# Performance work log

Measured on AMD Instinct MI355X. Metric: run time of the kernel, lower is better.

The kernel has to match this reference:

```python
import jax, jax.numpy as jnp
import numpy as np

N_NODES = 50000
N_EDGES = 800000
IN_F, HID, NCLS = 128, 64, 64
N_EXTRA = 2          # layer - 2
K_STEPS = 10
ALPHA = 0.1
BN_EPS = 1e-5


def setup_inputs() -> dict:
    key = jax.random.key(0)
    ks = jax.random.split(key, 20)
    d = {}
    d['x'] = jax.random.normal(ks[0], (N_NODES, IN_F), dtype=jnp.float32)
    d['edge_index'] = jax.random.randint(ks[1], (2, N_EDGES), 0, N_NODES, dtype=jnp.int64)
    s = 1.0 / np.sqrt(HID)
    d['W1'] = jax.random.normal(ks[2], (IN_F, HID), dtype=jnp.float32) / np.sqrt(IN_F)
    d['b1'] = jnp.zeros((HID,), jnp.float32)
    d['W2'] = jax.random.normal(ks[3], (HID, HID), dtype=jnp.float32) * s
    d['b2'] = jnp.zeros((HID,), jnp.float32)
    d['Wx'] = jax.random.normal(ks[4], (N_EXTRA, HID, HID), dtype=jnp.float32) * s
    d['bx'] = jnp.zeros((N_EXTRA, HID), jnp.float32)
    d['g1'] = jnp.ones((HID,), jnp.float32); d['be1'] = jnp.zeros((HID,), jnp.float32)
    d['g2'] = jnp.ones((HID,), jnp.float32); d['be2'] = jnp.zeros((HID,), jnp.float32)
    d['g3'] = jnp.ones((HID,), jnp.float32); d['be3'] = jnp.zeros((HID,), jnp.float32)
    d['Wfc'] = jax.random.normal(ks[5], (HID, NCLS), dtype=jnp.float32) * s
    d['bfc'] = jnp.zeros((NCLS,), jnp.float32)
    return d


def _gcn_norm(edge_index, n):
    # add self-loops, symmetric D^-1/2 (A+I) D^-1/2 normalization (PyG GCNConv default)
    loop = jnp.arange(n, dtype=edge_index.dtype)
    src = jnp.concatenate([edge_index[0], loop])
    dst = jnp.concatenate([edge_index[1], loop])
    deg = jax.ops.segment_sum(jnp.ones(src.shape[0], jnp.float32), dst, num_segments=n)
    dinv = jnp.where(deg > 0, jax.lax.rsqrt(deg), 0.0)
    return src, dst, dinv[src] * dinv[dst]


def _propagate(x, src, dst, w, n):
    # gather-scale-scatter: out[dst] += w * x[src]
    return jax.ops.segment_sum(x[src] * w[:, None], dst, num_segments=n)


def _bn(x, g, b):
    # BatchNorm1d in training mode: batch statistics over the node dim
    m = jnp.mean(x, axis=0)
    v = jnp.var(x, axis=0)
    return g * (x - m) * jax.lax.rsqrt(v + BN_EPS) + b


def reference(x, edge_index, W1, b1, W2, b2, Wx, bx, g1, be1, g2, be2, g3, be3, Wfc, bfc):
    n = x.shape[0]
    src, dst, w = _gcn_norm(edge_index, n)
    h = _propagate(x @ W1, src, dst, w, n) + b1
    h = jax.nn.relu(_bn(h, g1, be1))
    h = _propagate(h @ W2, src, dst, w, n) + b2
    h = jax.nn.relu(_bn(h, g2, be2))
    for i in range(Wx.shape[0]):
        h = _propagate(h @ Wx[i], src, dst, w, n) + bx[i]
        h = jax.nn.relu(_bn(h, g3, be3))
    # APPNP: K power-iteration steps with teleport back to h0
    h0 = h
    for _ in range(K_STEPS):
        h = (1.0 - ALPHA) * _propagate(h, src, dst, w, n) + ALPHA * h0
    out = h @ Wfc + bfc
    return jax.nn.log_softmax(out, axis=1)
```

## Files before the change

### kernel.cpp

```cpp
#include <hip/hip_runtime.h>
#include <hip/hip_fp16.h>
#include <cstdint>
#include <cstddef>

#define NN 50000
#define NE 800000
#define HID 64
#define INF_ 128
#define BN_EPS 1e-5f
#define NGRP (NN / 8)
#define NG16 (NN / 16)
#define SCAN_B 196
#define NSLICE 32
#define NBKT 16

typedef float floatx2 __attribute__((ext_vector_type(2)));

__device__ __forceinline__ float4 h8_to_f4(float2 raw) {
    union { float f; __half2 h; } ua, ub;
    ua.f = raw.x; ub.f = raw.y;
    float2 fa = __half22float2(ua.h), fb = __half22float2(ub.h);
    return make_float4(fa.x, fa.y, fb.x, fb.y);
}
__device__ __forceinline__ float2 f4_to_h8(float4 v) {
    union { float f; __half2 h; } ua, ub;
    ua.h = __float22half2_rn(make_float2(v.x, v.y));
    ub.h = __float22half2_rn(make_float2(v.z, v.w));
    return make_float2(ua.f, ub.f);
}
struct f8 { float v[8]; };
__device__ __forceinline__ f8 h16_to_f8(float4 raw) {
    f8 r;
    union { float f; __half2 h; } u;
    float2 a;
    u.f = raw.x; a = __half22float2(u.h); r.v[0] = a.x; r.v[1] = a.y;
    u.f = raw.y; a = __half22float2(u.h); r.v[2] = a.x; r.v[3] = a.y;
    u.f = raw.z; a = __half22float2(u.h); r.v[4] = a.x; r.v[5] = a.y;
    u.f = raw.w; a = __half22float2(u.h); r.v[6] = a.x; r.v[7] = a.y;
    return r;
}
__device__ __forceinline__ float4 f8_to_h16(const f8& s) {
    union { float f; __half2 h; } u;
    float4 o;
    u.h = __float22half2_rn(make_float2(s.v[0], s.v[1])); o.x = u.f;
    u.h = __float22half2_rn(make_float2(s.v[2], s.v[3])); o.y = u.f;
    u.h = __float22half2_rn(make_float2(s.v[4], s.v[5])); o.z = u.f;
    u.h = __float22half2_rn(make_float2(s.v[6], s.v[7])); o.w = u.f;
    return o;
}

__device__ __forceinline__ void fp8x8_to_f(unsigned lo, unsigned hi, float out[8]) {
    floatx2 a = __builtin_amdgcn_cvt_pk_f32_fp8((int)lo, false);
    floatx2 b = __builtin_amdgcn_cvt_pk_f32_fp8((int)lo, true);
    floatx2 c = __builtin_amdgcn_cvt_pk_f32_fp8((int)hi, false);
    floatx2 d = __builtin_amdgcn_cvt_pk_f32_fp8((int)hi, true);
    out[0] = a[0]; out[1] = a[1]; out[2] = b[0]; out[3] = b[1];
    out[4] = c[0]; out[5] = c[1]; out[6] = d[0]; out[7] = d[1];
}
__device__ __forceinline__ void fp8x16_to_f(uint4 r, float out[16]) {
    fp8x8_to_f(r.x, r.y, out);
    fp8x8_to_f(r.z, r.w, out + 8);
}
__device__ __forceinline__ uint2 f_to_fp8x8(const float v[8]) {
    int w0 = __builtin_amdgcn_cvt_pk_fp8_f32(v[0], v[1], 0, false);
    w0 = __builtin_amdgcn_cvt_pk_fp8_f32(v[2], v[3], w0, true);
    int w1 = __builtin_amdgcn_cvt_pk_fp8_f32(v[4], v[5], 0, false);
    w1 = __builtin_amdgcn_cvt_pk_fp8_f32(v[6], v[7], w1, true);
    uint2 o; o.x = (unsigned)w0; o.y = (unsigned)w1;
    return o;
}
__device__ __forceinline__ uint4 f_to_fp8x16(const float v[16]) {
    uint2 a = f_to_fp8x8(v), b = f_to_fp8x8(v + 8);
    uint4 o; o.x = a.x; o.y = a.y; o.z = b.x; o.w = b.y;
    return o;
}


__global__ void count_k(const int* __restrict__ dst, int* __restrict__ cnt) {
    int e = blockIdx.x * blockDim.x + threadIdx.x;
    if (e < NE) atomicAdd(&cnt[dst[e]], 1);
}

__global__ void dinv_k(const int* __restrict__ cnt, float* __restrict__ dinv) {
    int n = blockIdx.x * blockDim.x + threadIdx.x;
    if (n < NN) dinv[n] = rsqrtf((float)(cnt[n] + 1));
}

__global__ void zrow_k(float4* __restrict__ tmpH, uint4* __restrict__ x8a,
                       uint4* __restrict__ x8b) {
    int t = threadIdx.x;
    if (t < 8) tmpH[(size_t)NN * 8 + t] = make_float4(0.f, 0.f, 0.f, 0.f);
    else if (t < 12) x8a[(size_t)NN * 4 + (t - 8)] = make_uint4(0, 0, 0, 0);
    else if (t < 16) x8b[(size_t)NN * 4 + (t - 12)] = make_uint4(0, 0, 0, 0);
}

__global__ void scan1_k(const int* __restrict__ cnt, int* __restrict__ offs,
                        int* __restrict__ bsum) {
    __shared__ int sh[256];
    int t = threadIdx.x, i = blockIdx.x * 256 + t;
    int v = (i < NN) ? ((cnt[i] + 7) & ~7) : 0;
    sh[t] = v;
    __syncthreads();
    for (int d = 1; d < 256; d <<= 1) {
        int u = (t >= d) ? sh[t - d] : 0;
        __syncthreads();
        sh[t] += u;
        __syncthreads();
    }
    if (i < NN) offs[i] = sh[t] - v;
    if (t == 255) bsum[blockIdx.x] = sh[255];
}

__global__ void scan2_k(const int* __restrict__ bsum, int* __restrict__ bpre,
                        int* __restrict__ offs) {
    __shared__ int sh[256];
    int t = threadIdx.x;
    int v = (t < SCAN_B) ? bsum[t] : 0;
    sh[t] = v;
    __syncthreads();
    for (int d = 1; d < 256; d <<= 1) {
        int u = (t >= d) ? sh[t - d] : 0;
        __syncthreads();
        sh[t] += u;
        __syncthreads();
    }
    bpre[t] = sh[t] - v;
    if (t == 255) offs[NN] = sh[255];
}

__global__ void scan3_k(int* __restrict__ offs, const int* __restrict__ bpre) {
    int i = blockIdx.x * blockDim.x + threadIdx.x;
    if (i < NN) offs[i] += bpre[i >> 8];
}

__global__ void pad_k(const int* __restrict__ cnt, const int* __restrict__ offs,
                      int* __restrict__ edge1) {
    int n = blockIdx.x * blockDim.x + threadIdx.x;
    if (n >= NN) return;
    int e = offs[n] + cnt[n], e1 = offs[n + 1];
    for (; e < e1; ++e) edge1[e] = NN;
}

__global__ void scatter_k(const int* __restrict__ src, const int* __restrict__ dst,
                          const int* __restrict__ offs, int* __restrict__ cursor,
                          int* __restrict__ edge1) {
    int e = blockIdx.x * blockDim.x + threadIdx.x;
    if (e < NE) {
        int d = dst[e];
        int pos = offs[d] + atomicAdd(&cursor[d], 1);
        edge1[pos] = src[e];
    }
}

__global__ void hist_k(const int* __restrict__ cnt, int* __restrict__ hist) {
    __shared__ int lh[NBKT];
    int t = threadIdx.x;
    if (t < NBKT) lh[t] = 0;
    __syncthreads();
    int n = blockIdx.x * 256 + t;
    if (n < NN) {
        int c = (cnt[n] + 7) >> 3;
        if (c > NBKT - 1) c = NBKT - 1;
        atomicAdd(&lh[c], 1);
    }
    __syncthreads();
    if (t < NBKT && lh[t]) atomicAdd(&hist[t], lh[t]);
}

__global__ void scan16_k(const int* __restrict__ hist, int* __restrict__ bcur) {
    if (threadIdx.x == 0) {
        int s = 0;
        for (int i = 0; i < NBKT; ++i) { bcur[i] = s; s += hist[i]; }
    }
}

__global__ void perm_k(const int* __restrict__ cnt, int* __restrict__ bcur,
                       int* __restrict__ perm) {
    __shared__ int lh[NBKT], lbase[NBKT];
    int t = threadIdx.x;
    if (t < NBKT) lh[t] = 0;
    __syncthreads();
    int n = blockIdx.x * 256 + t;
    int c = 0, r = 0;
    if (n < NN) {
        c = (cnt[n] + 7) >> 3;
        if (c > NBKT - 1) c = NBKT - 1;
        r = atomicAdd(&lh[c], 1);
    }
    __syncthreads();
    if (t < NBKT) lbase[t] = lh[t] ? atomicAdd(&bcur[t], lh[t]) : 0;
    __syncthreads();
    if (n < NN) perm[lbase[c] + r] = n;
}

template <int K, bool HIN>
__global__ __launch_bounds__(256, 2) void mm_k(const void* __restrict__ Xv,
                                               const float* __restrict__ W,
                                               const float* __restrict__ dinv,
                                               float2* __restrict__ Y) {
    constexpr int RS = K + 4;
    __shared__ float Xs[64 * RS];
    __shared__ float Ws[K * 64];
    const int t = threadIdx.x;
    const int n0 = blockIdx.x * 64;

    {
        const float4* Wg = (const float4*)W;
        for (int g2 = t; g2 < K * 16; g2 += 256) {
            int row = g2 >> 4, c4 = g2 & 15;
            *(float4*)&Ws[row * 64 + c4 * 4] = Wg[g2];
        }
    }
    if (HIN) {
        const float4* Xg = (const float4*)Xv;
        for (int g2 = t; g2 < 64 * (K / 8); g2 += 256) {
            int row = g2 / (K / 8), c8 = g2 % (K / 8);
            int rr = n0 + row; if (rr >= NN) rr = NN - 1;
            f8 v = h16_to_f8(Xg[(size_t)rr * (K / 8) + c8]);
            float* dp = &Xs[row * RS + c8 * 8];
#pragma unroll
            for (int j = 0; j < 8; ++j) dp[j] = v.v[j];
        }
    } else {
        const float4* Xg = (const float4*)Xv;
        for (int g2 = t; g2 < 64 * (K / 4); g2 += 256) {
            int row = g2 / (K / 4), c4 = g2 % (K / 4);
            int rr = n0 + row; if (rr >= NN) rr = NN - 1;
            *(float4*)&Xs[row * RS + c4 * 4] = Xg[(size_t)rr * (K / 4) + c4];
        }
    }
    __syncthreads();

    const int r0 = (t >> 4) << 2;
    const int c0 = (t & 15) << 2;
    float acc[4][4];
#pragma unroll
    for (int j = 0; j < 4; ++j)
#pragma unroll
        for (int c = 0; c < 4; ++c) acc[j][c] = 0.f;

#pragma unroll 8
    for (int kq = 0; kq < K / 4; ++kq) {
        float4 xv[4];
#pragma unroll
        for (int j = 0; j < 4; ++j)
            xv[j] = *(const float4*)&Xs[(r0 + j) * RS + kq * 4];
        float4 wv[4];
#pragma unroll
        for (int i = 0; i < 4; ++i)
            wv[i] = *(const float4*)&Ws[(kq * 4 + i) * 64 + c0];
#pragma unroll
        for (int j = 0; j < 4; ++j) {
            acc[j][0] = fmaf(xv[j].x, wv[0].x, acc[j][0]);
            acc[j][1] = fmaf(xv[j].x, wv[0].y, acc[j][1]);
            acc[j][2] = fmaf(xv[j].x, wv[0].z, acc[j][2]);
            acc[j][3] = fmaf(xv[j].x, wv[0].w, acc[j][3]);
            acc[j][0] = fmaf(xv[j].y, wv[1].x, acc[j][0]);
            acc[j][1] = fmaf(xv[j].y, wv[1].y, acc[j][1]);
            acc[j][2] = fmaf(xv[j].y, wv[1].z, acc[j][2]);
            acc[j][3] = fmaf(xv[j].y, wv[1].w, acc[j][3]);
            acc[j][0] = fmaf(xv[j].z, wv[2].x, acc[j][0]);
            acc[j][1] = fmaf(xv[j].z, wv[2].y, acc[j][1]);
            acc[j][2] = fmaf(xv[j].z, wv[2].z, acc[j][2]);
            acc[j][3] = fmaf(xv[j].z, wv[2].w, acc[j][3]);
            acc[j][0] = fmaf(xv[j].w, wv[3].x, acc[j][0]);
            acc[j][1] = fmaf(xv[j].w, wv[3].y, acc[j][1]);
            acc[j][2] = fmaf(xv[j].w, wv[3].z, acc[j][2]);
            acc[j][3] = fmaf(xv[j].w, wv[3].w, acc[j][3]);
        }
    }

#pragma unroll
    for (int j = 0; j < 4; ++j) {
        int rr = n0 + r0 + j;
        if (rr < NN) {
            float dn = dinv[rr];
            Y[(size_t)rr * 16 + (t & 15)] =
                f4_to_h8(make_float4(acc[j][0] * dn, acc[j][1] * dn,
                                     acc[j][2] * dn, acc[j][3] * dn));
        }
    }
}

__device__ __forceinline__ void prop_gather8(const float4* __restrict__ X4,
                                             const int* __restrict__ E,
                                             int e0, int e1, int fl, int slotbase,
                                             float acc[8]) {
    if (e0 >= e1) return;
    int d = E[e0 + fl];
    float4 ra[4];
#pragma unroll
    for (int i = 0; i < 4; ++i) {
        int s = __shfl(d, slotbase + i, 64);
        ra[i] = X4[(size_t)s * 8 + fl];
    }
    for (int e = e0; e < e1; e += 8) {
        float4 rb[4];
#pragma unroll
        for (int i = 0; i < 4; ++i) {
            int s = __shfl(d, slotbase + 4 + i, 64);
            rb[i] = X4[(size_t)s * 8 + fl];
        }
        bool more = (e + 8 < e1);
        if (more) d = E[e + 8 + fl];
        __builtin_amdgcn_sched_barrier(0);
#pragma unroll
        for (int i = 0; i < 4; ++i) {
            f8 x = h16_to_f8(ra[i]);
#pragma unroll
            for (int j = 0; j < 8; ++j) acc[j] += x.v[j];
        }
        if (more) {
#pragma unroll
            for (int i = 0; i < 4; ++i) {
                int s = __shfl(d, slotbase + i, 64);
                ra[i] = X4[(size_t)s * 8 + fl];
            }
        }
        __builtin_amdgcn_sched_barrier(0);
#pragma unroll
        for (int i = 0; i < 4; ++i) {
            f8 x = h16_to_f8(rb[i]);
#pragma unroll
            for (int j = 0; j < 8; ++j) acc[j] += x.v[j];
        }
    }
}

__global__ __launch_bounds__(256, 3) void prop_stats_k(
        const float4* __restrict__ X4, const int* __restrict__ offs,
        const int* __restrict__ edge1, const float* __restrict__ dinv,
        const float* __restrict__ bias, const int* __restrict__ perm,
        float4* __restrict__ Y4, float* __restrict__ stats) {
    const int lane = threadIdx.x & 63;
    const int wave = threadIdx.x >> 6;
    const int slot = lane >> 3;
    const int fl = lane & 7;
    const int slotbase = lane & 56;
    const int wid = blockIdx.x * 4 + wave;
    const int nw = gridDim.x * 4;

    float bias8[8];
    {
        float4 b0 = ((const float4*)bias)[fl * 2];
        float4 b1 = ((const float4*)bias)[fl * 2 + 1];
        bias8[0] = b0.x; bias8[1] = b0.y; bias8[2] = b0.z; bias8[3] = b0.w;
        bias8[4] = b1.x; bias8[5] = b1.y; bias8[6] = b1.z; bias8[7] = b1.w;
    }

    float s1[8], s2[8];
#pragma unroll
    for (int j = 0; j < 8; ++j) { s1[j] = 0.f; s2[j] = 0.f; }

    for (int g = wid; g < NGRP; g += nw) {
        int n = perm[g * 8 + slot];
        float dn = dinv[n];
        f8 self = h16_to_f8(X4[(size_t)n * 8 + fl]);
        float acc[8];
#pragma unroll
        for (int j = 0; j < 8; ++j) acc[j] = self.v[j];
        int e0 = offs[n], e1 = offs[n + 1];
        prop_gather8(X4, edge1, e0, e1, fl, slotbase, acc);
        f8 o;
#pragma unroll
        for (int j = 0; j < 8; ++j) {
            float a = fmaf(dn, acc[j], bias8[j]);
            o.v[j] = a;
            s1[j] += a;
            s2[j] = fmaf(a, a, s2[j]);
        }
        Y4[(size_t)n * 8 + fl] = f8_to_h16(o);
    }

#pragma unroll
    for (int m = 8; m <= 32; m <<= 1) {
#pragma unroll
        for (int j = 0; j < 8; ++j) {
            s1[j] += __shfl_xor(s1[j], m, 64);
            s2[j] += __shfl_xor(s2[j], m, 64);
        }
    }

    __shared__ float red[4][8][16];
    if (lane < 8) {
#pragma unroll
        for (int j = 0; j < 8; ++j) {
            red[wave][lane][j] = s1[j];
            red[wave][lane][8 + j] = s2[j];
        }
    }
    __syncthreads();
    int t = threadIdx.x;
    if (t < 128) {
        int j = t & 63;
        int isq = t >> 6;
        int fli = j >> 3, c = (j & 7) + isq * 8;
        float a = red[0][fli][c] + red[1][fli][c] + red[2][fli][c] + red[3][fli][c];
        atomicAdd(&stats[(blockIdx.x & (NSLICE - 1)) * 128 + isq * 64 + j], a);
    }
}

template <bool EMIT8>
__global__ __launch_bounds__(256) void bn_relu_k(
        const float4* __restrict__ Y4, const float* __restrict__ slices,
        const float* __restrict__ g, const float* __restrict__ be,
        float4* __restrict__ H4, uint2* __restrict__ X8,
        const float* __restrict__ dinv) {
    __shared__ float fs[128];
    int t = threadIdx.x;
    if (t < 128) {
        float s = 0.f;
#pragma unroll
        for (int k = 0; k < NSLICE; ++k) s += slices[k * 128 + t];
        fs[t] = s;
    }
    __syncthreads();
    int i = blockIdx.x * blockDim.x + t;
    if (i >= NN * 8) return;
    int fg = i & 7;
    const float invN = 1.f / (float)NN;
    f8 y = h16_to_f8(Y4[i]);
    float4 gv0 = ((const float4*)g)[fg * 2];
    float4 gv1 = ((const float4*)g)[fg * 2 + 1];
    float4 bv0 = ((const float4*)be)[fg * 2];
    float4 bv1 = ((const float4*)be)[fg * 2 + 1];
    float gv[8] = { gv0.x, gv0.y, gv0.z, gv0.w, gv1.x, gv1.y, gv1.z, gv1.w };
    float bv[8] = { bv0.x, bv0.y, bv0.z, bv0.w, bv1.x, bv1.y, bv1.z, bv1.w };
    f8 o;
#pragma unroll
    for (int j = 0; j < 8; ++j) {
        float m = fs[fg * 8 + j] * invN;
        float v = fs[64 + fg * 8 + j] * invN - m * m;
        float val = fmaf(gv[j] * rsqrtf(v + BN_EPS), y.v[j] - m, bv[j]);
        o.v[j] = val > 0.f ? val : 0.f;
    }
    H4[i] = f8_to_h16(o);
    if (EMIT8) {
        float dn = dinv[i >> 3];
        float sv[8];
#pragma unroll
        for (int j = 0; j < 8; ++j) sv[j] = dn * o.v[j];
        X8[i] = f_to_fp8x8(sv);
    }
}

template <bool OUT16>
__global__ __launch_bounds__(256, 3) void appnp8_k(
        const uint4* __restrict__ X8, const float4* __restrict__ H04,
        const int* __restrict__ offs, const int* __restrict__ edge1,
        const float* __restrict__ dinv, const int* __restrict__ perm,
        uint4* __restrict__ Y8, float4* __restrict__ Y16) {
    const int lane = threadIdx.x & 63;
    const int wave = threadIdx.x >> 6;
    const int slot = lane >> 2;
    const int fl = lane & 3;
    const int quadbase = lane & 60;
    const int wid = blockIdx.x * 4 + wave;
    if (wid >= NG16) return;
    int n = perm[wid * 16 + slot];
    float dn = dinv[n];
    float acc[16];
    {
        float self[16];
        fp8x16_to_f(X8[(size_t)n * 4 + fl], self);
#pragma unroll
        for (int j = 0; j < 16; ++j) acc[j] = self[j];
    }
    int e0 = offs[n], e1 = offs[n + 1];
    if (e0 < e1) {
        int2 d = ((const int2*)(edge1 + e0))[fl];
        uint4 ra[4];
#pragma unroll
        for (int k = 0; k < 4; ++k) {
            int s = __shfl((k & 1) ? d.y : d.x, quadbase + (k >> 1), 64);
            ra[k] = X8[(size_t)s * 4 + fl];
        }
        for (int e = e0; e < e1; e += 8) {
            uint4 rb[4];
#pragma unroll
            for (int k = 0; k < 4; ++k) {
                int s = __shfl((k & 1) ? d.y : d.x, quadbase + 2 + (k >> 1), 64);
                rb[k] = X8[(size_t)s * 4 + fl];
            }
            bool more = (e + 8 < e1);
            if (more) d = ((const int2*)(edge1 + e + 8))[fl];
            __builtin_amdgcn_sched_barrier(0);
#pragma unroll
            for (int k = 0; k < 4; ++k) {
                float x[16];
                fp8x16_to_f(ra[k], x);
#pragma unroll
                for (int j = 0; j < 16; ++j) acc[j] += x[j];
            }
            if (more) {
#pragma unroll
                for (int k = 0; k < 4; ++k) {
                    int s = __shfl((k & 1) ? d.y : d.x, quadbase + (k >> 1), 64);
                    ra[k] = X8[(size_t)s * 4 + fl];
                }
            }
            __builtin_amdgcn_sched_barrier(0);
#pragma unroll
            for (int k = 0; k < 4; ++k) {
                float x[16];
                fp8x16_to_f(rb[k], x);
#pragma unroll
                for (int j = 0; j < 16; ++j) acc[j] += x[j];
            }
        }
    }
    f8 ha = h16_to_f8(H04[(size_t)n * 8 + fl * 2]);
    f8 hb = h16_to_f8(H04[(size_t)n * 8 + fl * 2 + 1]);
    float o[16];
    float s = 0.9f * dn;
#pragma unroll
    for (int j = 0; j < 8; ++j) {
        o[j] = fmaf(s, acc[j], 0.1f * ha.v[j]);
        o[8 + j] = fmaf(s, acc[8 + j], 0.1f * hb.v[j]);
    }
    if (OUT16) {
        f8 lo, hi;
#pragma unroll
        for (int j = 0; j < 8; ++j) { lo.v[j] = o[j]; hi.v[j] = o[8 + j]; }
        Y16[(size_t)n * 8 + fl * 2] = f8_to_h16(lo);
        Y16[(size_t)n * 8 + fl * 2 + 1] = f8_to_h16(hi);
    } else {
        float so[16];
#pragma unroll
        for (int j = 0; j < 16; ++j) so[j] = dn * o[j];
        Y8[(size_t)n * 4 + fl] = f_to_fp8x16(so);
    }
}

__global__ __launch_bounds__(256) void final_k(const float2* __restrict__ H2,
                                               const float* __restrict__ Wfc,
                                               const float* __restrict__ bfc,
                                               float* __restrict__ out) {
    const int t = threadIdx.x;
    const int n0 = blockIdx.x * 64;
    const int r0 = (t >> 4) << 2;
    const int c0 = (t & 15) << 2;

    int r[4];
#pragma unroll
    for (int j = 0; j < 4; ++j) {
        int rr = n0 + r0 + j;
        r[j] = rr < NN ? rr : NN - 1;
    }
    const float2* Xr[4];
#pragma unroll
    for (int j = 0; j < 4; ++j) Xr[j] = H2 + (size_t)r[j] * 16;

    float4 bf = *(const float4*)(bfc + c0);
    float acc[4][4];
#pragma unroll
    for (int j = 0; j < 4; ++j) {
        acc[j][0] = bf.x; acc[j][1] = bf.y; acc[j][2] = bf.z; acc[j][3] = bf.w;
    }

#pragma unroll 4
    for (int kq = 0; kq < 16; ++kq) {
        float4 xv[4];
#pragma unroll
        for (int j = 0; j < 4; ++j) xv[j] = h8_to_f4(Xr[j][kq]);
        float4 wv[4];
#pragma unroll
        for (int i = 0; i < 4; ++i)
            wv[i] = *(const float4*)(Wfc + (size_t)(kq * 4 + i) * 64 + c0);
#pragma unroll
        for (int j = 0; j < 4; ++j) {
            acc[j][0] = fmaf(xv[j].x, wv[0].x, acc[j][0]);
            acc[j][1] = fmaf(xv[j].x, wv[0].y, acc[j][1]);
            acc[j][2] = fmaf(xv[j].x, wv[0].z, acc[j][2]);
            acc[j][3] = fmaf(xv[j].x, wv[0].w, acc[j][3]);
            acc[j][0] = fmaf(xv[j].y, wv[1].x, acc[j][0]);
            acc[j][1] = fmaf(xv[j].y, wv[1].y, acc[j][1]);
            acc[j][2] = fmaf(xv[j].y, wv[1].z, acc[j][2]);
            acc[j][3] = fmaf(xv[j].y, wv[1].w, acc[j][3]);
            acc[j][0] = fmaf(xv[j].z, wv[2].x, acc[j][0]);
            acc[j][1] = fmaf(xv[j].z, wv[2].y, acc[j][1]);
            acc[j][2] = fmaf(xv[j].z, wv[2].z, acc[j][2]);
            acc[j][3] = fmaf(xv[j].z, wv[2].w, acc[j][3]);
            acc[j][0] = fmaf(xv[j].w, wv[3].x, acc[j][0]);
            acc[j][1] = fmaf(xv[j].w, wv[3].y, acc[j][1]);
            acc[j][2] = fmaf(xv[j].w, wv[3].z, acc[j][2]);
            acc[j][3] = fmaf(xv[j].w, wv[3].w, acc[j][3]);
        }
    }

#pragma unroll
    for (int j = 0; j < 4; ++j) {
        float m = fmaxf(fmaxf(acc[j][0], acc[j][1]), fmaxf(acc[j][2], acc[j][3]));
#pragma unroll
        for (int d = 1; d <= 8; d <<= 1) m = fmaxf(m, __shfl_xor(m, d, 64));
        float s = expf(acc[j][0] - m) + expf(acc[j][1] - m) +
                  expf(acc[j][2] - m) + expf(acc[j][3] - m);
#pragma unroll
        for (int d = 1; d <= 8; d <<= 1) s += __shfl_xor(s, d, 64);
        float lse = m + logf(s);
        int rr = n0 + r0 + j;
        if (rr < NN)
            *(float4*)(out + (size_t)rr * 64 + c0) =
                make_float4(acc[j][0] - lse, acc[j][1] - lse,
                            acc[j][2] - lse, acc[j][3] - lse);
    }
}


static inline char* alignup(char* p, size_t a) {
    return (char*)(((uintptr_t)p + a - 1) & ~(uintptr_t)(a - 1));
}

extern "C" void kernel_launch(void* const* d_in, const int* in_sizes, int n_in,
                              void* d_out, int out_size, void* d_ws, size_t ws_size,
                              hipStream_t stream) {
    const float* x   = (const float*)d_in[0];
    const int*   ei  = (const int*)d_in[1];
    const float* W1  = (const float*)d_in[2];
    const float* b1  = (const float*)d_in[3];
    const float* W2  = (const float*)d_in[4];
    const float* b2  = (const float*)d_in[5];
    const float* Wx  = (const float*)d_in[6];
    const float* bx  = (const float*)d_in[7];
    const float* g1  = (const float*)d_in[8];
    const float* be1 = (const float*)d_in[9];
    const float* g2  = (const float*)d_in[10];
    const float* be2 = (const float*)d_in[11];
    const float* g3  = (const float*)d_in[12];
    const float* be3 = (const float*)d_in[13];
    const float* Wfc = (const float*)d_in[14];
    const float* bfc = (const float*)d_in[15];
    float* out = (float*)d_out;

    const int* srcA = ei;
    const int* dstA = ei + NE;

    char* p = (char*)d_ws;
    int*   deg    = (int*)p;   p += NN * 4;
    int*   cursor = (int*)p;   p += NN * 4;
    float* stats  = (float*)p; p += 4 * NSLICE * 128 * 4;
    int*   hist   = (int*)p;   p += NBKT * 4;
    size_t zbytes = (size_t)(p - (char*)d_ws);
    p = alignup(p, 512);
    int*   offs  = (int*)p;    p += (NN + 4) * 4;   p = alignup(p, 512);
    float* dinv  = (float*)p;  p += NN * 4;         p = alignup(p, 512);
    int*   bsum  = (int*)p;    p += 256 * 4;
    int*   bpre  = (int*)p;    p += 256 * 4;
    int*   bcur  = (int*)p;    p += NBKT * 4;       p = alignup(p, 512);
    int*   perm  = (int*)p;    p += NN * 4;         p = alignup(p, 512);
    int*   edge1 = (int*)p;    p += ((size_t)NE + 8 * NN + 256) * 4; p = alignup(p, 512);
    float4* tmpH = (float4*)p; p += ((size_t)NN + 1) * 128; p = alignup(p, 512);
    float4* hbH  = (float4*)p; p += (size_t)NN * 128;       p = alignup(p, 512);
    float4* apH  = (float4*)p; p += (size_t)NN * 128;       p = alignup(p, 512);
    float4* pbH  = (float4*)p; p += (size_t)NN * 128;       p = alignup(p, 512);
    uint4*  x8a  = (uint4*)p;  p += ((size_t)NN + 1) * 64;  p = alignup(p, 512);
    uint4*  x8b  = (uint4*)p;  p += ((size_t)NN + 1) * 64;

    hipMemsetAsync(d_ws, 0, zbytes, stream);

    count_k<<<(NE + 255) / 256, 256, 0, stream>>>(dstA, deg);
    dinv_k<<<(NN + 255) / 256, 256, 0, stream>>>(deg, dinv);
    zrow_k<<<1, 64, 0, stream>>>(tmpH, x8a, x8b);
    hist_k<<<SCAN_B, 256, 0, stream>>>(deg, hist);
    scan16_k<<<1, 64, 0, stream>>>(hist, bcur);
    perm_k<<<SCAN_B, 256, 0, stream>>>(deg, bcur, perm);
    scan1_k<<<SCAN_B, 256, 0, stream>>>(deg, offs, bsum);
    scan2_k<<<1, 256, 0, stream>>>(bsum, bpre, offs);
    scan3_k<<<(NN + 255) / 256, 256, 0, stream>>>(offs, bpre);
    pad_k<<<(NN + 255) / 256, 256, 0, stream>>>(deg, offs, edge1);
    scatter_k<<<(NE + 255) / 256, 256, 0, stream>>>(srcA, dstA, offs, cursor, edge1);

    const int MMG = (NN + 63) / 64;
    const int PG  = (NGRP + 3) / 4;
    const int AG  = (NG16 + 3) / 4;
    const int BNG = (NN * 8 + 255) / 256;
    const int SL  = NSLICE * 128;

    mm_k<INF_, false><<<MMG, 256, 0, stream>>>(x, W1, dinv, (float2*)tmpH);
    prop_stats_k<<<PG, 256, 0, stream>>>(tmpH, offs, edge1, dinv, b1, perm, pbH, stats + 0 * SL);
    bn_relu_k<false><<<BNG, 256, 0, stream>>>(pbH, stats + 0 * SL, g1, be1, hbH, nullptr, dinv);

    mm_k<HID, true><<<MMG, 256, 0, stream>>>(hbH, W2, dinv, (float2*)tmpH);
    prop_stats_k<<<PG, 256, 0, stream>>>(tmpH, offs, edge1, dinv, b2, perm, pbH, stats + 1 * SL);
    bn_relu_k<false><<<BNG, 256, 0, stream>>>(pbH, stats + 1 * SL, g2, be2, hbH, nullptr, dinv);

    mm_k<HID, true><<<MMG, 256, 0, stream>>>(hbH, Wx + (size_t)0 * 64 * 64, dinv, (float2*)tmpH);
    prop_stats_k<<<PG, 256, 0, stream>>>(tmpH, offs, edge1, dinv, bx + (size_t)0 * 64, perm,
                                         pbH, stats + 2 * SL);
    bn_relu_k<false><<<BNG, 256, 0, stream>>>(pbH, stats + 2 * SL, g3, be3, hbH, nullptr, dinv);

    mm_k<HID, true><<<MMG, 256, 0, stream>>>(hbH, Wx + (size_t)1 * 64 * 64, dinv, (float2*)tmpH);
    prop_stats_k<<<PG, 256, 0, stream>>>(tmpH, offs, edge1, dinv, bx + (size_t)1 * 64, perm,
                                         pbH, stats + 3 * SL);
    bn_relu_k<true><<<BNG, 256, 0, stream>>>(pbH, stats + 3 * SL, g3, be3, hbH, (uint2*)x8a, dinv);

    const uint4* cur8 = x8a;
    for (int it = 0; it < 9; ++it) {
        uint4* o8 = (cur8 == x8a) ? x8b : x8a;
        appnp8_k<false><<<AG, 256, 0, stream>>>(cur8, hbH, offs, edge1, dinv, perm, o8, nullptr);
        cur8 = o8;
    }
    appnp8_k<true><<<AG, 256, 0, stream>>>(cur8, hbH, offs, edge1, dinv, perm, nullptr, apH);

    final_k<<<MMG, 256, 0, stream>>>((const float2*)apH, Wfc, bfc, out);
}
```

Before: 496.8 us.

## Fuse ten APPNP hops into one cooperative persistent kernel with grid sync

Replaces ten separate APPNP propagation launches with one cooperative kernel of 512 persistent blocks. Each block loops over node groups and the blocks separate hops with a grid-wide sync, ping-ponging between the two fp8 buffers. This removes per-launch overhead and the tail drain between hops. In exchange it adds grid-barrier cost and lowers occupancy, since launch bounds go to 2 blocks per SM and the grid is fixed, and it falls back to the old launches if the cooperative launch fails.

Measured after the change: 1.855 ms. 273% more time.

```diff
diff --git a/kernel.cpp b/kernel.cpp
--- a/kernel.cpp
+++ b/kernel.cpp
@@ -1,5 +1,6 @@
 #include <hip/hip_runtime.h>
 #include <hip/hip_fp16.h>
+#include <hip/hip_cooperative_groups.h>
 #include <cstdint>
 #include <cstddef>
 
@@ -13,6 +14,9 @@
 #define SCAN_B 196
 #define NSLICE 32
 #define NBKT 16
+#define COOP_B 512
+
+namespace cg = cooperative_groups;
 
 typedef float floatx2 __attribute__((ext_vector_type(2)));
 
@@ -444,6 +448,87 @@
     }
 }
 
+__device__ __forceinline__ void appnp_hop(
+        const uint4* __restrict__ X8, uint4* __restrict__ Y8,
+        const float4* __restrict__ H04, const int* __restrict__ offs,
+        const int* __restrict__ edge1, const float* __restrict__ dinv,
+        const int* __restrict__ perm, float4* __restrict__ Y16,
+        bool out16, int wid, int slot, int fl, int quadbase) {
+    int n = perm[wid * 16 + slot];
+    float dn = dinv[n];
+    float acc[16];
+    {
+        float self[16];
+        fp8x16_to_f(X8[(size_t)n * 4 + fl], self);
+#pragma unroll
+        for (int j = 0; j < 16; ++j) acc[j] = self[j];
+    }
+    int e0 = offs[n], e1 = offs[n + 1];
+    if (e0 < e1) {
+        int2 d = ((const int2*)(edge1 + e0))[fl];
+        uint4 ra[4];
+#pragma unroll
+        for (int k = 0; k < 4; ++k) {
+            int s = __shfl((k & 1) ? d.y : d.x, quadbase + (k >> 1), 64);
+            ra[k] = X8[(size_t)s * 4 + fl];
+        }
+        for (int e = e0; e < e1; e += 8) {
+            uint4 rb[4];
+#pragma unroll
+            for (int k = 0; k < 4; ++k) {
+                int s = __shfl((k & 1) ? d.y : d.x, quadbase + 2 + (k >> 1), 64);
+                rb[k] = X8[(size_t)s * 4 + fl];
+            }
+            bool more = (e + 8 < e1);
+            if (more) d = ((const int2*)(edge1 + e + 8))[fl];
+            __builtin_amdgcn_sched_barrier(0);
+#pragma unroll
+            for (int k = 0; k < 4; ++k) {
+                float x[16];
+                fp8x16_to_f(ra[k], x);
+#pragma unroll
+                for (int j = 0; j < 16; ++j) acc[j] += x[j];
+            }
+            if (more) {
+#pragma unroll
+                for (int k = 0; k < 4; ++k) {
+                    int s = __shfl((k & 1) ? d.y : d.x, quadbase + (k >> 1), 64);
+                    ra[k] = X8[(size_t)s * 4 + fl];
+                }
+            }
+            __builtin_amdgcn_sched_barrier(0);
+#pragma unroll
+            for (int k = 0; k < 4; ++k) {
+                float x[16];
+                fp8x16_to_f(rb[k], x);
+#pragma unroll
+                for (int j = 0; j < 16; ++j) acc[j] += x[j];
+            }
+        }
+    }
+    f8 ha = h16_to_f8(H04[(size_t)n * 8 + fl * 2]);
+    f8 hb = h16_to_f8(H04[(size_t)n * 8 + fl * 2 + 1]);
+    float o[16];
+    float s = 0.9f * dn;
+#pragma unroll
+    for (int j = 0; j < 8; ++j) {
+        o[j] = fmaf(s, acc[j], 0.1f * ha.v[j]);
+        o[8 + j] = fmaf(s, acc[8 + j], 0.1f * hb.v[j]);
+    }
+    if (out16) {
+        f8 lo, hi;
+#pragma unroll
+        for (int j = 0; j < 8; ++j) { lo.v[j] = o[j]; hi.v[j] = o[8 + j]; }
+        Y16[(size_t)n * 8 + fl * 2] = f8_to_h16(lo);
+        Y16[(size_t)n * 8 + fl * 2 + 1] = f8_to_h16(hi);
+    } else {
+        float so[16];
+#pragma unroll
+        for (int j = 0; j < 16; ++j) so[j] = dn * o[j];
+        Y8[(size_t)n * 4 + fl] = f_to_fp8x16(so);
+    }
+}
+
 template <bool OUT16>
 __global__ __launch_bounds__(256, 3) void appnp8_k(
         const uint4* __restrict__ X8, const float4* __restrict__ H04,
@@ -452,83 +537,39 @@
         uint4* __restrict__ Y8, float4* __restrict__ Y16) {
     const int lane = threadIdx.x & 63;
     const int wave = threadIdx.x >> 6;
+    const int wid = blockIdx.x * 4 + wave;
+    if (wid >= NG16) return;
+    appnp_hop(X8, Y8, H04, offs, edge1, dinv, perm, Y16, OUT16,
+              wid, lane >> 2, lane & 3, lane & 60);
+}
+
+__global__ __launch_bounds__(256, 2) void appnp_fused_k(
+        uint4* __restrict__ x8a, uint4* __restrict__ x8b,
+        const float4* __restrict__ H04,
+        const int* __restrict__ offs, const int* __restrict__ edge1,
+        const float* __restrict__ dinv, const int* __restrict__ perm,
+        float4* __restrict__ Y16) {
+    cg::grid_group grid = cg::this_grid();
+    const int lane = threadIdx.x & 63;
+    const int wave = threadIdx.x >> 6;
     const int slot = lane >> 2;
     const int fl = lane & 3;
     const int quadbase = lane & 60;
-    const int wid = blockIdx.x * 4 + wave;
-    if (wid >= NG16) return;
-    int n = perm[wid * 16 + slot];
-    float dn = dinv[n];
-    float acc[16];
-    {
-        float self[16];
-        fp8x16_to_f(X8[(size_t)n * 4 + fl], self);
-#pragma unroll
-        for (int j = 0; j < 16; ++j) acc[j] = self[j];
-    }
-    int e0 = offs[n], e1 = offs[n + 1];
-    if (e0 < e1) {
-        int2 d = ((const int2*)(edge1 + e0))[fl];
-        uint4 ra[4];
-#pragma unroll
-        for (int k = 0; k < 4; ++k) {
-            int s = __shfl((k & 1) ? d.y : d.x, quadbase + (k >> 1), 64);
-            ra[k] = X8[(size_t)s * 4 + fl];
-        }
-        for (int e = e0; e < e1; e += 8) {
-            uint4 rb[4];
-#pragma unroll
-            for (int k = 0; k < 4; ++k) {
-                int s = __shfl((k & 1) ? d.y : d.x, quadbase + 2 + (k >> 1), 64);
-                rb[k] = X8[(size_t)s * 4 + fl];
-            }
-            bool more = (e + 8 < e1);
-            if (more) d = ((const int2*)(edge1 + e + 8))[fl];
-            __builtin_amdgcn_sched_barrier(0);
-#pragma unroll
-            for (int k = 0; k < 4; ++k) {
-                float x[16];
-                fp8x16_to_f(ra[k], x);
-#pragma unroll
-                for (int j = 0; j < 16; ++j) acc[j] += x[j];
-            }
-            if (more) {
-#pragma unroll
-                for (int k = 0; k < 4; ++k) {
-                    int s = __shfl((k & 1) ? d.y : d.x, quadbase + (k >> 1), 64);
-                    ra[k] = X8[(size_t)s * 4 + fl];
-                }
-            }
-            __builtin_amdgcn_sched_barrier(0);
-#pragma unroll
-            for (int k = 0; k < 4; ++k) {
-                float x[16];
-                fp8x16_to_f(rb[k], x);
-#pragma unroll
-                for (int j = 0; j < 16; ++j) acc[j] += x[j];
-            }
-        }
-    }
-    f8 ha = h16_to_f8(H04[(size_t)n * 8 + fl * 2]);
-    f8 hb = h16_to_f8(H04[(size_t)n * 8 + fl * 2 + 1]);
-    float o[16];
-    float s = 0.9f * dn;
-#pragma unroll
-    for (int j = 0; j < 8; ++j) {
-        o[j] = fmaf(s, acc[j], 0.1f * ha.v[j]);
-        o[8 + j] = fmaf(s, acc[8 + j], 0.1f * hb.v[j]);
-    }
-    if (OUT16) {
-        f8 lo, hi;
-#pragma unroll
-        for (int j = 0; j < 8; ++j) { lo.v[j] = o[j]; hi.v[j] = o[8 + j]; }
-        Y16[(size_t)n * 8 + fl * 2] = f8_to_h16(lo);
-        Y16[(size_t)n * 8 + fl * 2 + 1] = f8_to_h16(hi);
-    } else {
-        float so[16];
-#pragma unroll
-        for (int j = 0; j < 16; ++j) so[j] = dn * o[j];
-        Y8[(size_t)n * 4 + fl] = f_to_fp8x16(so);
+    const int wid0 = blockIdx.x * 4 + wave;
+    const int nw = gridDim.x * 4;
+
+    for (int hop = 0; hop < 10; ++hop) {
+        const uint4* X8 = (hop & 1) ? x8b : x8a;
+        uint4* Y8 = (hop & 1) ? x8a : x8b;
+        const bool out16 = (hop == 9);
+        for (int wid = wid0; wid < NG16; wid += nw)
+            appnp_hop(X8, Y8, H04, offs, edge1, dinv, perm, Y16, out16,
+                      wid, slot, fl, quadbase);
+        if (hop < 9) {
+            __threadfence();
+            grid.sync();
+            __threadfence();
+        }
     }
 }
 
@@ -694,13 +735,27 @@
                                          pbH, stats + 3 * SL);
     bn_relu_k<true><<<BNG, 256, 0, stream>>>(pbH, stats + 3 * SL, g3, be3, hbH, (uint2*)x8a, dinv);
 
-    const uint4* cur8 = x8a;
-    for (int it = 0; it < 9; ++it) {
-        uint4* o8 = (cur8 == x8a) ? x8b : x8a;
-        appnp8_k<false><<<AG, 256, 0, stream>>>(cur8, hbH, offs, edge1, dinv, perm, o8, nullptr);
-        cur8 = o8;
-    }
-    appnp8_k<true><<<AG, 256, 0, stream>>>(cur8, hbH, offs, edge1, dinv, perm, nullptr, apH);
+    {
+        uint4* pa = x8a; uint4* pb = x8b;
+        const float4* ph = hbH;
+        const int* po = offs; const int* pe = edge1;
+        const float* pd = dinv; const int* pp = perm;
+        float4* py = apH;
+        void* cargs[] = { &pa, &pb, &ph, &po, &pe, &pd, &pp, &py };
+        hipError_t cerr = hipLaunchCooperativeKernel(
+            (const void*)appnp_fused_k, dim3(COOP_B), dim3(256), cargs, 0, stream);
+        if (cerr != hipSuccess) {
+            const uint4* cur8 = x8a;
+            for (int it = 0; it < 9; ++it) {
+                uint4* o8 = (cur8 == x8a) ? x8b : x8a;
+                appnp8_k<false><<<AG, 256, 0, stream>>>(cur8, hbH, offs, edge1,
+                                                        dinv, perm, o8, nullptr);
+                cur8 = o8;
+            }
+            appnp8_k<true><<<AG, 256, 0, stream>>>(cur8, hbH, offs, edge1,
+                                                   dinv, perm, nullptr, apH);
+        }
+    }
 
     final_k<<<MMG, 256, 0, stream>>>((const float2*)apH, Wfc, bfc, out);
 }
```

## Fuse BatchNorm-ReLU into next matmul and bin-sort edges for CSR build

Applied to the files above, without the earlier changes.

Replaces the per-edge global-atomic scatter for building the CSR with a two-pass binned counting sort. Edges are first grouped into 256-node bins through shared-memory staging, then placed per bin using shared-memory cursors. It also fuses the BN+ReLU of the first three GCN layers into a new mm_bn_k kernel, so the intermediate normalized activations are no longer written out and read back. The cost is an extra pairs buffer and more kernel launches for the sort.

New measurement: 476.4 us. -4.1%, faster.

```diff
diff --git a/kernel.cpp b/kernel.cpp
--- a/kernel.cpp
+++ b/kernel.cpp
@@ -13,6 +13,8 @@
 #define SCAN_B 196
 #define NSLICE 32
 #define NBKT 16
+#define NBIN 196
+#define EPB 2048
 
 typedef float floatx2 __attribute__((ext_vector_type(2)));
 
@@ -141,14 +143,99 @@
     for (; e < e1; ++e) edge1[e] = NN;
 }
 
-__global__ void scatter_k(const int* __restrict__ src, const int* __restrict__ dst,
-                          const int* __restrict__ offs, int* __restrict__ cursor,
-                          int* __restrict__ edge1) {
-    int e = blockIdx.x * blockDim.x + threadIdx.x;
-    if (e < NE) {
-        int d = dst[e];
-        int pos = offs[d] + atomicAdd(&cursor[d], 1);
-        edge1[pos] = src[e];
+__global__ void binhist_k(const int* __restrict__ cnt, int* __restrict__ bincnt) {
+    __shared__ int sh[256];
+    int b = blockIdx.x, t = threadIdx.x;
+    int n = b * 256 + t;
+    sh[t] = (n < NN) ? cnt[n] : 0;
+    __syncthreads();
+    for (int d = 128; d > 0; d >>= 1) {
+        if (t < d) sh[t] += sh[t + d];
+        __syncthreads();
+    }
+    if (t == 0) bincnt[b] = sh[0];
+}
+
+__global__ void scanbin_k(const int* __restrict__ bincnt, int* __restrict__ boffs,
+                          int* __restrict__ bcur) {
+    __shared__ int sh[256];
+    int t = threadIdx.x;
+    int v = (t < NBIN) ? bincnt[t] : 0;
+    sh[t] = v;
+    __syncthreads();
+    for (int d = 1; d < 256; d <<= 1) {
+        int u = (t >= d) ? sh[t - d] : 0;
+        __syncthreads();
+        sh[t] += u;
+        __syncthreads();
+    }
+    boffs[t] = sh[t] - v;
+    bcur[t] = sh[t] - v;
+    if (t == 255) boffs[NBIN] = sh[255];
+}
+
+__global__ __launch_bounds__(256) void binscat_k(
+        const int* __restrict__ src, const int* __restrict__ dst,
+        int* __restrict__ bcur, int2* __restrict__ pairs) {
+    __shared__ int lcnt[256], lscan[256], lexc[256], gbase[256];
+    __shared__ int2 stage[EPB];
+    const int t = threadIdx.x;
+    const int base = blockIdx.x * EPB;
+    lcnt[t] = 0;
+    __syncthreads();
+    int2 mypair[EPB / 256];
+    int mybin[EPB / 256], myr[EPB / 256];
+#pragma unroll
+    for (int i = 0; i < EPB / 256; ++i) {
+        int e = base + i * 256 + t;
+        if (e < NE) {
+            int s = src[e], d = dst[e];
+            mypair[i] = make_int2(s, d);
+            mybin[i] = d >> 8;
+            myr[i] = atomicAdd(&lcnt[mybin[i]], 1);
+        } else mybin[i] = -1;
+    }
+    __syncthreads();
+    lscan[t] = lcnt[t];
+    __syncthreads();
+    for (int d = 1; d < 256; d <<= 1) {
+        int u = (t >= d) ? lscan[t - d] : 0;
+        __syncthreads();
+        lscan[t] += u;
+        __syncthreads();
+    }
+    lexc[t] = lscan[t] - lcnt[t];
+    if (lcnt[t] > 0) gbase[t] = atomicAdd(&bcur[t], lcnt[t]);
+    __syncthreads();
+#pragma unroll
+    for (int i = 0; i < EPB / 256; ++i)
+        if (mybin[i] >= 0) stage[lexc[mybin[i]] + myr[i]] = mypair[i];
+    __syncthreads();
+    const int total = lscan[255];
+#pragma unroll
+    for (int i = 0; i < EPB / 256; ++i) {
+        int s = i * 256 + t;
+        if (s < total) {
+            int2 pr = stage[s];
+            int b = pr.y >> 8;
+            pairs[(size_t)gbase[b] + (s - lexc[b])] = pr;
+        }
+    }
+}
+
+__global__ __launch_bounds__(256) void binplace_k(
+        const int* __restrict__ boffs, const int2* __restrict__ pairs,
+        const int* __restrict__ offs, int* __restrict__ edge1) {
+    __shared__ int lcur[256];
+    const int b = blockIdx.x, t = threadIdx.x;
+    lcur[t] = 0;
+    __syncthreads();
+    int s0 = boffs[b], s1 = boffs[b + 1];
+    for (int s = s0 + t; s < s1; s += 256) {
+        int2 pr = pairs[s];
+        int d = pr.y;
+        int slot = atomicAdd(&lcur[d & 255], 1);
+        edge1[offs[d] + slot] = pr.x;
     }
 }
 
@@ -282,6 +369,105 @@
     }
 }
 
+__global__ __launch_bounds__(256, 2) void mm_bn_k(
+        const float4* __restrict__ Y4in, const float* __restrict__ slices,
+        const float* __restrict__ gg, const float* __restrict__ be,
+        const float* __restrict__ W, const float* __restrict__ dinv,
+        float2* __restrict__ Y) {
+    constexpr int K = 64, RS = K + 4;
+    __shared__ float Xs[64 * RS];
+    __shared__ float Ws[K * 64];
+    __shared__ float fs[128], gs[64], bs[64];
+    const int t = threadIdx.x;
+    const int n0 = blockIdx.x * 64;
+
+    if (t < 128) {
+        float s = 0.f;
+#pragma unroll
+        for (int k = 0; k < NSLICE; ++k) s += slices[k * 128 + t];
+        fs[t] = s;
+    } else if (t < 192) {
+        gs[t - 128] = gg[t - 128];
+    } else {
+        bs[t - 192] = be[t - 192];
+    }
+    {
+        const float4* Wg = (const float4*)W;
+        for (int g2 = t; g2 < K * 16; g2 += 256) {
+            int row = g2 >> 4, c4 = g2 & 15;
+            *(float4*)&Ws[row * 64 + c4 * 4] = Wg[g2];
+        }
+    }
+    __syncthreads();
+
+    const float invN = 1.f / (float)NN;
+    for (int g2 = t; g2 < 64 * 8; g2 += 256) {
+        int row = g2 >> 3, c8 = g2 & 7;
+        int rr = n0 + row; if (rr >= NN) rr = NN - 1;
+        f8 v = h16_to_f8(Y4in[(size_t)rr * 8 + c8]);
+        float* dp = &Xs[row * RS + c8 * 8];
+#pragma unroll
+        for (int j = 0; j < 8; ++j) {
+            int f = c8 * 8 + j;
+            float m = fs[f] * invN;
+            float va = fs[64 + f] * invN - m * m;
+            float val = fmaf(gs[f] * rsqrtf(va + BN_EPS), v.v[j] - m, bs[f]);
+            dp[j] = val > 0.f ? val : 0.f;
+        }
+    }
+    __syncthreads();
+
+    const int r0 = (t >> 4) << 2;
+    const int c0 = (t & 15) << 2;
+    float acc[4][4];
+#pragma unroll
+    for (int j = 0; j < 4; ++j)
+#pragma unroll
+        for (int c = 0; c < 4; ++c) acc[j][c] = 0.f;
+
+#pragma unroll 8
+    for (int kq = 0; kq < K / 4; ++kq) {
+        float4 xv[4];
+#pragma unroll
+        for (int j = 0; j < 4; ++j)
+            xv[j] = *(const float4*)&Xs[(r0 + j) * RS + kq * 4];
+        float4 wv[4];
+#pragma unroll
+        for (int i = 0; i < 4; ++i)
+            wv[i] = *(const float4*)&Ws[(kq * 4 + i) * 64 + c0];
+#pragma unroll
+        for (int j = 0; j < 4; ++j) {
+            acc[j][0] = fmaf(xv[j].x, wv[0].x, acc[j][0]);
+            acc[j][1] = fmaf(xv[j].x, wv[0].y, acc[j][1]);
+            acc[j][2] = fmaf(xv[j].x, wv[0].z, acc[j][2]);
+            acc[j][3] = fmaf(xv[j].x, wv[0].w, acc[j][3]);
+            acc[j][0] = fmaf(xv[j].y, wv[1].x, acc[j][0]);
+            acc[j][1] = fmaf(xv[j].y, wv[1].y, acc[j][1]);
+            acc[j][2] = fmaf(xv[j].y, wv[1].z, acc[j][2]);
+            acc[j][3] = fmaf(xv[j].y, wv[1].w, acc[j][3]);
+            acc[j][0] = fmaf(xv[j].z, wv[2].x, acc[j][0]);
+            acc[j][1] = fmaf(xv[j].z, wv[2].y, acc[j][1]);
+            acc[j][2] = fmaf(xv[j].z, wv[2].z, acc[j][2]);
+            acc[j][3] = fmaf(xv[j].z, wv[2].w, acc[j][3]);
+            acc[j][0] = fmaf(xv[j].w, wv[3].x, acc[j][0]);
+            acc[j][1] = fmaf(xv[j].w, wv[3].y, acc[j][1]);
+            acc[j][2] = fmaf(xv[j].w, wv[3].z, acc[j][2]);
+            acc[j][3] = fmaf(xv[j].w, wv[3].w, acc[j][3]);
+        }
+    }
+
+#pragma unroll
+    for (int j = 0; j < 4; ++j) {
+        int rr = n0 + r0 + j;
+        if (rr < NN) {
+            float dn = dinv[rr];
+            Y[(size_t)rr * 16 + (t & 15)] =
+                f4_to_h8(make_float4(acc[j][0] * dn, acc[j][1] * dn,
+                                     acc[j][2] * dn, acc[j][3] * dn));
+        }
+    }
+}
+
 __device__ __forceinline__ void prop_gather8(const float4* __restrict__ X4,
                                              const int* __restrict__ E,
                                              int e0, int e1, int fl, int slotbase,
@@ -400,7 +586,6 @@
     }
 }
 
-template <bool EMIT8>
 __global__ __launch_bounds__(256) void bn_relu_k(
         const float4* __restrict__ Y4, const float* __restrict__ slices,
         const float* __restrict__ g, const float* __restrict__ be,
@@ -435,7 +620,7 @@
         o.v[j] = val > 0.f ? val : 0.f;
     }
     H4[i] = f8_to_h16(o);
-    if (EMIT8) {
+    {
         float dn = dinv[i >> 3];
         float sv[8];
 #pragma unroll
@@ -637,7 +822,6 @@
 
     char* p = (char*)d_ws;
     int*   deg    = (int*)p;   p += NN * 4;
-    int*   cursor = (int*)p;   p += NN * 4;
     float* stats  = (float*)p; p += 4 * NSLICE * 128 * 4;
     int*   hist   = (int*)p;   p += NBKT * 4;
     size_t zbytes = (size_t)(p - (char*)d_ws);
@@ -646,9 +830,13 @@
     float* dinv  = (float*)p;  p += NN * 4;         p = alignup(p, 512);
     int*   bsum  = (int*)p;    p += 256 * 4;
     int*   bpre  = (int*)p;    p += 256 * 4;
-    int*   bcur  = (int*)p;    p += NBKT * 4;       p = alignup(p, 512);
+    int*   bcur  = (int*)p;    p += NBKT * 4;
+    int*   bincnt = (int*)p;   p += 256 * 4;
+    int*   bbcur  = (int*)p;   p += 256 * 4;
+    int*   boffs  = (int*)p;   p += 260 * 4;        p = alignup(p, 512);
     int*   perm  = (int*)p;    p += NN * 4;         p = alignup(p, 512);
     int*   edge1 = (int*)p;    p += ((size_t)NE + 8 * NN + 256) * 4; p = alignup(p, 512);
+    int2*  pairs = (int2*)p;   p += (size_t)NE * 8; p = alignup(p, 512);
     float4* tmpH = (float4*)p; p += ((size_t)NN + 1) * 128; p = alignup(p, 512);
     float4* hbH  = (float4*)p; p += (size_t)NN * 128;       p = alignup(p, 512);
     float4* apH  = (float4*)p; p += (size_t)NN * 128;       p = alignup(p, 512);
@@ -668,7 +856,10 @@
     scan2_k<<<1, 256, 0, stream>>>(bsum, bpre, offs);
     scan3_k<<<(NN + 255) / 256, 256, 0, stream>>>(offs, bpre);
     pad_k<<<(NN + 255) / 256, 256, 0, stream>>>(deg, offs, edge1);
-    scatter_k<<<(NE + 255) / 256, 256, 0, stream>>>(srcA, dstA, offs, cursor, edge1);
+    binhist_k<<<NBIN, 256, 0, stream>>>(deg, bincnt);
+    scanbin_k<<<1, 256, 0, stream>>>(bincnt, boffs, bbcur);
+    binscat_k<<<(NE + EPB - 1) / EPB, 256, 0, stream>>>(srcA, dstA, bbcur, pairs);
+    binplace_k<<<NBIN, 256, 0, stream>>>(boffs, pairs, offs, edge1);
 
     const int MMG = (NN + 63) / 64;
     const int PG  = (NGRP + 3) / 4;
@@ -678,21 +869,15 @@
 
     mm_k<INF_, false><<<MMG, 256, 0, stream>>>(x, W1, dinv, (float2*)tmpH);
     prop_stats_k<<<PG, 256, 0, stream>>>(tmpH, offs, edge1, dinv, b1, perm, pbH, stats + 0 * SL);
-    bn_relu_k<false><<<BNG, 256, 0, stream>>>(pbH, stats + 0 * SL, g1, be1, hbH, nullptr, dinv);
-
-    mm_k<HID, true><<<MMG, 256, 0, stream>>>(hbH, W2, dinv, (float2*)tmpH);
+    mm_bn_k<<<MMG, 256, 0, stream>>>(pbH, stats + 0 * SL, g1, be1, W2, dinv, (float2*)tmpH);
     prop_stats_k<<<PG, 256, 0, stream>>>(tmpH, offs, edge1, dinv, b2, perm, pbH, stats + 1 * SL);
-    bn_relu_k<false><<<BNG, 256, 0, stream>>>(pbH, stats + 1 * SL, g2, be2, hbH, nullptr, dinv);
-
-    mm_k<HID, true><<<MMG, 256, 0, stream>>>(hbH, Wx + (size_t)0 * 64 * 64, dinv, (float2*)tmpH);
-    prop_stats_k<<<PG, 256, 0, stream>>>(tmpH, offs, edge1, dinv, bx + (size_t)0 * 64, perm,
-                                         pbH, stats + 2 * SL);
-    bn_relu_k<false><<<BNG, 256, 0, stream>>>(pbH, stats + 2 * SL, g3, be3, hbH, nullptr, dinv);
-
-    mm_k<HID, true><<<MMG, 256, 0, stream>>>(hbH, Wx + (size_t)1 * 64 * 64, dinv, (float2*)tmpH);
-    prop_stats_k<<<PG, 256, 0, stream>>>(tmpH, offs, edge1, dinv, bx + (size_t)1 * 64, perm,
+    mm_bn_k<<<MMG, 256, 0, stream>>>(pbH, stats + 1 * SL, g2, be2, Wx, dinv, (float2*)tmpH);
+    prop_stats_k<<<PG, 256, 0, stream>>>(tmpH, offs, edge1, dinv, bx, perm, pbH, stats + 2 * SL);
+    mm_bn_k<<<MMG, 256, 0, stream>>>(pbH, stats + 2 * SL, g3, be3,
+                                     Wx + (size_t)64 * 64, dinv, (float2*)tmpH);
+    prop_stats_k<<<PG, 256, 0, stream>>>(tmpH, offs, edge1, dinv, bx + 64, perm,
                                          pbH, stats + 3 * SL);
-    bn_relu_k<true><<<BNG, 256, 0, stream>>>(pbH, stats + 3 * SL, g3, be3, hbH, (uint2*)x8a, dinv);
+    bn_relu_k<<<BNG, 256, 0, stream>>>(pbH, stats + 3 * SL, g3, be3, hbH, (uint2*)x8a, dinv);
 
     const uint4* cur8 = x8a;
     for (int it = 0; it < 9; ++it) {
```
